# Optimization experiments

Hardware: AMD Instinct MI355X
Metric: run time of the kernel (lower is better)

Reference implementation:

```python
import jax, jax.numpy as jnp
import numpy as np

B = 4096
T = 66            # total_char_ids = 51 + 8 + 6 + 1
EMB = 128
ITEM_EMB = 64     # emb_dim // 2
NUM_ITEMS = 287
ITEMS_IN_GAME = 70  # 7 * 10
N_SCREEN = 24
N_MINI = 40
CONT = 32


def _unique_ids(key, batch, n):
    keys = jax.random.split(key, batch)
    return jax.vmap(lambda k: jax.random.permutation(k, T)[:n])(keys).astype(jnp.int32)


def setup_inputs() -> dict:
    key = jax.random.key(0)
    ks = jax.random.split(key, 16)
    inp = {
        "continuous_f": jax.random.normal(ks[0], (B, CONT), jnp.float32),
        "screen_feats": jax.random.uniform(ks[1], (B, N_SCREEN, 4), jnp.float32),
        "minimap_feats": jax.random.uniform(ks[2], (B, N_MINI, 2), jnp.float32),
        "char_emb": jax.random.normal(ks[3], (T, EMB), jnp.float32) * 0.02,
        "item_emb": jax.random.normal(ks[4], (NUM_ITEMS, ITEM_EMB), jnp.float32) * 0.02,
        "Ws1": jax.random.normal(ks[5], (EMB + 4, EMB), jnp.float32) * 0.05,
        "bs1": jnp.zeros((EMB,), jnp.float32),
        "Ws2": jax.random.normal(ks[6], (EMB, EMB), jnp.float32) * 0.05,
        "bs2": jnp.zeros((EMB,), jnp.float32),
        "Wm1": jax.random.normal(ks[7], (EMB + 2, EMB), jnp.float32) * 0.05,
        "bm1": jnp.zeros((EMB,), jnp.float32),
        "Wm2": jax.random.normal(ks[8], (EMB, EMB), jnp.float32) * 0.05,
        "bm2": jnp.zeros((EMB,), jnp.float32),
        "screen_ids": _unique_ids(ks[9], B, N_SCREEN),
        "minimap_ids": _unique_ids(ks[10], B, N_MINI),
        "items": jax.random.randint(ks[11], (B, ITEMS_IN_GAME), 0, NUM_ITEMS, jnp.int32),
    }
    return inp


def reference(continuous_f, screen_feats, minimap_feats, char_emb, item_emb,
              Ws1, bs1, Ws2, bs2, Wm1, bm1, Wm2, bm2,
              screen_ids, minimap_ids, items):
    b = continuous_f.shape[0]
    rows = jnp.arange(b)[:, None]

    # scatter detections by char id into fixed [T, .] buffers (vectorized over batch)
    scr = jnp.zeros((b, T, 4), screen_feats.dtype).at[rows, screen_ids].set(screen_feats)
    mini = jnp.zeros((b, T, 2), minimap_feats.dtype).at[rows, minimap_ids].set(minimap_feats)

    # item embedding lookup -> [b, 70*64]
    item_flat = item_emb[items].reshape(b, -1)

    base = jnp.broadcast_to(char_emb, (b, T, EMB))  # all char ids embedded

    def mlp(x, W1, b1, W2, b2):
        h = jax.nn.relu(jnp.einsum('btf,fh->bth', x, W1) + b1)
        return jnp.einsum('bth,hk->btk', h, W2) + b2

    screen_out = mlp(jnp.concatenate([base, scr], axis=-1), Ws1, bs1, Ws2, bs2)
    mini_out = mlp(jnp.concatenate([base, mini], axis=-1), Wm1, bm1, Wm2, bm2)

    obs = jnp.concatenate(
        [continuous_f, screen_out.reshape(b, -1), mini_out.reshape(b, -1), item_flat],
        axis=-1)  # [b, 32 + 66*128 + 66*128 + 70*64] = [b, 21408]
    return obs
```

## Files before the change

### kernel.cpp

```cpp
#include <hip/hip_runtime.h>
#include <stdint.h>

#define BDIM 256
#define PDIM 512
#define T_   66
#define EMB  128
#define NS   24
#define NM   40
#define NBS  42
#define NBM  26
#define NI   70
#define CONT 32
#define OUTW 21408

typedef __attribute__((ext_vector_type(4))) float f32x4;
typedef __attribute__((ext_vector_type(8))) unsigned short u16x8;
typedef __attribute__((ext_vector_type(8))) __bf16 bf16x8;

static __device__ __forceinline__ unsigned short f2bf(float x) {
  union { float f; unsigned u; } v; v.f = x;
  unsigned r = (v.u + 0x7FFFu + ((v.u >> 16) & 1u)) >> 16;
  return (unsigned short)r;
}

static __device__ __forceinline__ f32x4 mfma16(u16x8 a, u16x8 b, f32x4 c) {
  return __builtin_amdgcn_mfma_f32_16x16x32_bf16(
      __builtin_bit_cast(bf16x8, a), __builtin_bit_cast(bf16x8, b), c, 0, 0, 0);
}

__global__ __launch_bounds__(PDIM) void precomp(
    const float* __restrict__ char_emb,
    const float* __restrict__ Ws1, const float* __restrict__ bs1,
    const float* __restrict__ Ws2, const float* __restrict__ bs2,
    const float* __restrict__ Wm1, const float* __restrict__ bm1,
    const float* __restrict__ Wm2, const float* __restrict__ bm2,
    float* __restrict__ base_h_s, float* __restrict__ base_h_m,
    float* __restrict__ base_out_s, float* __restrict__ base_out_m,
    unsigned short* __restrict__ w2s_swz, unsigned short* __restrict__ w2m_swz) {
  const int bb = blockIdx.x, tid = threadIdx.x;
  if (bb < T_) {
    const int t = bb;
    const int quarter = tid >> 7;
    const int col = tid & 127;
    const int mlp = quarter & 1;
    const int kh = quarter >> 1;
    const float* W1 = mlp ? Wm1 : Ws1;
    const float* W2 = mlp ? Wm2 : Ws2;
    const float* b1 = mlp ? bm1 : bs1;
    const float* b2 = mlp ? bm2 : bs2;
    float* bh = mlp ? base_h_m : base_h_s;
    float* bo = mlp ? base_out_m : base_out_s;
    __shared__ float part[4][EMB];
    __shared__ float h[2][EMB];
    float acc = 0.f;
#pragma unroll 8
    for (int f = kh * 64; f < kh * 64 + 64; ++f)
      acc += char_emb[t * EMB + f] * W1[f * EMB + col];
    part[quarter][col] = acc;
    __syncthreads();
    if (tid < 256) {
      const float v = b1[col] + part[mlp][col] + part[2 + mlp][col];
      bh[t * EMB + col] = v;
      h[mlp][col] = fmaxf(v, 0.f);
    }
    __syncthreads();
    float acc2 = 0.f;
#pragma unroll 8
    for (int i = kh * 64; i < kh * 64 + 64; ++i)
      acc2 += h[mlp][i] * W2[i * EMB + col];
    part[quarter][col] = acc2;
    __syncthreads();
    if (tid < 256)
      bo[t * EMB + col] = b2[col] + part[mlp][col] + part[2 + mlp][col];
  } else {
    const int mlp = bb - T_;
    const float* W2 = mlp ? Wm2 : Ws2;
    unsigned short* dst = mlp ? w2m_swz : w2s_swz;
    for (int idx = tid; idx < 8 * 4 * 64 * 8; idx += PDIM) {
      const int e = idx & 7, lane = (idx >> 3) & 63, kk = (idx >> 9) & 3, n = idx >> 11;
      const int k = kk * 32 + (lane >> 4) * 8 + e;
      const int col = n * 16 + (lane & 15);
      dst[idx] = f2bf(W2[k * EMB + col]);
    }
  }
}

__global__ __launch_bounds__(BDIM, 5) void fused(
    const float* __restrict__ contf,
    const float* __restrict__ sfeat,
    const float* __restrict__ mfeat,
    const float* __restrict__ item_emb,
    const float* __restrict__ Ws1,
    const float* __restrict__ bs2,
    const float* __restrict__ Wm1,
    const float* __restrict__ bm2,
    const int* __restrict__ sids,
    const int* __restrict__ mids,
    const int* __restrict__ items,
    const float* __restrict__ base_h_s, const float* __restrict__ base_h_m,
    const float* __restrict__ base_out_s, const float* __restrict__ base_out_m,
    const unsigned short* __restrict__ w2s_swz, const unsigned short* __restrict__ w2m_swz,
    float* __restrict__ out) {
  const int bid = blockIdx.x, tid = threadIdx.x;
  const int b = bid >> 1;

  __shared__ int s_id[NS], m_id[NM];
  __shared__ float s_f[NS * 4], m_f[NM * 2];
  __shared__ u16x8 h_frag[5 * 4 * 64];
  __shared__ int s_map[T_], m_map[T_];
  __shared__ int listS[T_], listM[T_], s_item[NI];
  __shared__ int cntS, cntM;

  float* outS = out + (size_t)b * OUTW + CONT;
  float* outM = outS + T_ * EMB;

  if (bid & 1) {
    if (tid < NS) s_id[tid] = sids[b * NS + tid];
    if (tid < NM) m_id[tid] = mids[b * NM + tid];
    if (tid < NS * 4) s_f[tid] = sfeat[b * NS * 4 + tid];
    if (tid < NM * 2) m_f[tid] = mfeat[b * NM * 2 + tid];
    __syncthreads();

    for (int u = tid; u < 5 * 4 * 64; u += BDIM) {
      const int lane = u & 63, kk = (u >> 6) & 3, tile = u >> 8;
      const int g = lane >> 4, r = lane & 15;
      const int k0 = kk * 32 + g * 8;
      const bool scr = tile < 2;
      const int j = scr ? tile * 16 + r : (tile - 2) * 16 + r;
      const int nd = scr ? NS : NM;
      float v[8];
      if (j < nd) {
        const int t = scr ? s_id[j] : m_id[j];
        const float* bh = (scr ? base_h_s : base_h_m) + t * EMB + k0;
#pragma unroll
        for (int e = 0; e < 8; ++e) v[e] = bh[e];
        if (scr) {
          const float* fp = &s_f[j * 4];
#pragma unroll
          for (int c = 0; c < 4; ++c) {
            const float fc = fp[c];
            const float* wp = Ws1 + (128 + c) * EMB + k0;
#pragma unroll
            for (int e = 0; e < 8; ++e) v[e] += fc * wp[e];
          }
        } else {
          const float* fp = &m_f[j * 2];
#pragma unroll
          for (int c = 0; c < 2; ++c) {
            const float fc = fp[c];
            const float* wp = Wm1 + (128 + c) * EMB + k0;
#pragma unroll
            for (int e = 0; e < 8; ++e) v[e] += fc * wp[e];
          }
        }
#pragma unroll
        for (int e = 0; e < 8; ++e) v[e] = fmaxf(v[e], 0.f);
      } else {
#pragma unroll
        for (int e = 0; e < 8; ++e) v[e] = 0.f;
      }
      u16x8 pk;
#pragma unroll
      for (int e = 0; e < 8; ++e) pk[e] = f2bf(v[e]);
      h_frag[u] = pk;
    }
    __syncthreads();

    const int lane = tid & 63, w = tid >> 6;
    const int g = lane >> 4, r = lane & 15;
    const int n0 = w * 2;

    u16x8 bb[2][4];
    float bias[2];
#pragma unroll
    for (int n = 0; n < 2; ++n) {
      bias[n] = bs2[(n0 + n) * 16 + r];
#pragma unroll
      for (int kk = 0; kk < 4; ++kk)
        bb[n][kk] = reinterpret_cast<const u16x8*>(w2s_swz)[((n0 + n) * 4 + kk) * 64 + lane];
    }
#pragma unroll
    for (int m = 0; m < 2; ++m) {
#pragma unroll
      for (int n = 0; n < 2; ++n) {
        f32x4 acc = {bias[n], bias[n], bias[n], bias[n]};
#pragma unroll
        for (int kk = 0; kk < 4; ++kk)
          acc = mfma16(h_frag[(m * 4 + kk) * 64 + lane], bb[n][kk], acc);
#pragma unroll
        for (int q = 0; q < 4; ++q) {
          const int rd = m * 16 + g * 4 + q;
          if (rd < NS) {
            const int t = s_id[rd];
            __builtin_nontemporal_store(acc[q], outS + t * EMB + (n0 + n) * 16 + r);
          }
        }
      }
    }
#pragma unroll
    for (int n = 0; n < 2; ++n) {
      bias[n] = bm2[(n0 + n) * 16 + r];
#pragma unroll
      for (int kk = 0; kk < 4; ++kk)
        bb[n][kk] = reinterpret_cast<const u16x8*>(w2m_swz)[((n0 + n) * 4 + kk) * 64 + lane];
    }
#pragma unroll
    for (int m = 0; m < 3; ++m) {
#pragma unroll
      for (int n = 0; n < 2; ++n) {
        f32x4 acc = {bias[n], bias[n], bias[n], bias[n]};
#pragma unroll
        for (int kk = 0; kk < 4; ++kk)
          acc = mfma16(h_frag[((m + 2) * 4 + kk) * 64 + lane], bb[n][kk], acc);
#pragma unroll
        for (int q = 0; q < 4; ++q) {
          const int rd = m * 16 + g * 4 + q;
          if (rd < NM) {
            const int t = m_id[rd];
            __builtin_nontemporal_store(acc[q], outM + t * EMB + (n0 + n) * 16 + r);
          }
        }
      }
    }
  } else {
    if (tid == 0) { cntS = 0; cntM = 0; }
    if (tid < T_) { s_map[tid] = -1; m_map[tid] = -1; }
    if (tid < NS) s_id[tid] = sids[b * NS + tid];
    if (tid < NM) m_id[tid] = mids[b * NM + tid];
    if (tid < NI) s_item[tid] = items[b * NI + tid];
    __syncthreads();
    if (tid < NS) s_map[s_id[tid]] = 1;
    if (tid < NM) m_map[m_id[tid]] = 1;
    __syncthreads();
    if (tid < T_ && s_map[tid] < 0) { const int p = atomicAdd(&cntS, 1); listS[p] = tid; }
    if (tid < T_ && m_map[tid] < 0) { const int p = atomicAdd(&cntM, 1); listM[p] = tid; }
    __syncthreads();

    if (tid < 8) {
      const f32x4 v = reinterpret_cast<const f32x4*>(contf + (size_t)b * CONT)[tid];
      __builtin_nontemporal_store(v, reinterpret_cast<f32x4*>(out + (size_t)b * OUTW) + tid);
    }
    for (int u = tid; u < NBS * 32; u += BDIM) {
      const int d = u >> 5, q = u & 31;
      const int t = listS[d];
      const f32x4 v = reinterpret_cast<const f32x4*>(base_out_s + t * EMB)[q];
      __builtin_nontemporal_store(v, reinterpret_cast<f32x4*>(outS + t * EMB) + q);
    }
    for (int u = tid; u < NBM * 32; u += BDIM) {
      const int d = u >> 5, q = u & 31;
      const int t = listM[d];
      const f32x4 v = reinterpret_cast<const f32x4*>(base_out_m + t * EMB)[q];
      __builtin_nontemporal_store(v, reinterpret_cast<f32x4*>(outM + t * EMB) + q);
    }
    float* outI = out + (size_t)b * OUTW + (CONT + 2 * T_ * EMB);
    for (int u = tid; u < NI * 16; u += BDIM) {
      const int j = u >> 4, q = u & 15;
      const int it = s_item[j];
      const f32x4 v = reinterpret_cast<const f32x4*>(item_emb + it * 64)[q];
      __builtin_nontemporal_store(v, reinterpret_cast<f32x4*>(outI + j * 64) + q);
    }
  }
}

extern "C" void kernel_launch(void* const* d_in, const int* in_sizes, int n_in,
                              void* d_out, int out_size, void* d_ws, size_t ws_size,
                              hipStream_t stream) {
  const float* contf    = (const float*)d_in[0];
  const float* sfeat    = (const float*)d_in[1];
  const float* mfeat    = (const float*)d_in[2];
  const float* char_emb = (const float*)d_in[3];
  const float* item_emb = (const float*)d_in[4];
  const float* Ws1 = (const float*)d_in[5];
  const float* bs1 = (const float*)d_in[6];
  const float* Ws2 = (const float*)d_in[7];
  const float* bs2 = (const float*)d_in[8];
  const float* Wm1 = (const float*)d_in[9];
  const float* bm1 = (const float*)d_in[10];
  const float* Wm2 = (const float*)d_in[11];
  const float* bm2 = (const float*)d_in[12];
  const int* sids  = (const int*)d_in[13];
  const int* mids  = (const int*)d_in[14];
  const int* items = (const int*)d_in[15];
  float* out = (float*)d_out;

  const int B = in_sizes[0] / CONT;

  char* ws = (char*)d_ws;
  float* base_h_s   = (float*)(ws + 0);
  float* base_h_m   = (float*)(ws + 33792);
  float* base_out_s = (float*)(ws + 67584);
  float* base_out_m = (float*)(ws + 101376);
  unsigned short* w2s = (unsigned short*)(ws + 135168);
  unsigned short* w2m = (unsigned short*)(ws + 167936);

  precomp<<<T_ + 2, PDIM, 0, stream>>>(char_emb, Ws1, bs1, Ws2, bs2, Wm1, bm1, Wm2, bm2,
                                       base_h_s, base_h_m, base_out_s, base_out_m, w2s, w2m);
  fused<<<2 * B, BDIM, 0, stream>>>(contf, sfeat, mfeat, item_emb, Ws1, bs2, Wm1, bm2,
                                    sids, mids, items,
                                    base_h_s, base_h_m, base_out_s, base_out_m, w2s, w2m, out);
}
```

Before: 122.4 us.

## Process four samples per block with double-buffered metadata and hoisted W2 fragments

Replaces the two-blocks-per-sample split (MLP block and copy block) with one block handling four consecutive samples. Per-sample ids and features are double-buffered in shared memory, so loading and building the next sample overlaps the stores of the current one, and the W2 MFMA fragments and biases are loaded into registers once per block. The base-row fill now checks a per-char map instead of using an atomic-built list. This cuts launch count and repeated weight loads but gives 4x fewer blocks, more registers (the occupancy hint was removed), and serialised work within each block.

```diff
diff --git a/kernel.cpp b/kernel.cpp
--- a/kernel.cpp
+++ b/kernel.cpp
@@ -3,12 +3,11 @@
 
 #define BDIM 256
 #define PDIM 512
+#define SPB  4
 #define T_   66
 #define EMB  128
 #define NS   24
 #define NM   40
-#define NBS  42
-#define NBM  26
 #define NI   70
 #define CONT 32
 #define OUTW 21408
@@ -85,7 +84,7 @@
   }
 }
 
-__global__ __launch_bounds__(BDIM, 5) void fused(
+__global__ __launch_bounds__(BDIM) void fused(
     const float* __restrict__ contf,
     const float* __restrict__ sfeat,
     const float* __restrict__ mfeat,
@@ -100,42 +99,63 @@
     const float* __restrict__ base_h_s, const float* __restrict__ base_h_m,
     const float* __restrict__ base_out_s, const float* __restrict__ base_out_m,
     const unsigned short* __restrict__ w2s_swz, const unsigned short* __restrict__ w2m_swz,
-    float* __restrict__ out) {
-  const int bid = blockIdx.x, tid = threadIdx.x;
-  const int b = bid >> 1;
-
-  __shared__ int s_id[NS], m_id[NM];
-  __shared__ float s_f[NS * 4], m_f[NM * 2];
-  __shared__ u16x8 h_frag[5 * 4 * 64];
-  __shared__ int s_map[T_], m_map[T_];
-  __shared__ int listS[T_], listM[T_], s_item[NI];
-  __shared__ int cntS, cntM;
-
-  float* outS = out + (size_t)b * OUTW + CONT;
-  float* outM = outS + T_ * EMB;
-
-  if (bid & 1) {
-    if (tid < NS) s_id[tid] = sids[b * NS + tid];
-    if (tid < NM) m_id[tid] = mids[b * NM + tid];
-    if (tid < NS * 4) s_f[tid] = sfeat[b * NS * 4 + tid];
-    if (tid < NM * 2) m_f[tid] = mfeat[b * NM * 2 + tid];
-    __syncthreads();
-
-    for (int u = tid; u < 5 * 4 * 64; u += BDIM) {
-      const int lane = u & 63, kk = (u >> 6) & 3, tile = u >> 8;
-      const int g = lane >> 4, r = lane & 15;
-      const int k0 = kk * 32 + g * 8;
+    float* __restrict__ out, int B) {
+  const int tid = threadIdx.x;
+  const int s0 = blockIdx.x * SPB;
+  const int nS = min(SPB, B - s0);
+  if (nS <= 0) return;
+
+  __shared__ u16x8 h_frag[2][5 * 4 * 64];
+  __shared__ int s_id[2][NS], m_id[2][NM], s_item[2][NI];
+  __shared__ int s_map[2][T_], m_map[2][T_];
+  __shared__ float s_f[2][NS * 4], m_f[2][NM * 2];
+
+  const int lane = tid & 63, w = tid >> 6;
+  const int g = lane >> 4, r = lane & 15;
+  const int n0 = w * 2;
+
+  u16x8 bS[2][4], bM[2][4];
+  float biasS[2], biasM[2];
+#pragma unroll
+  for (int n = 0; n < 2; ++n) {
+    biasS[n] = bs2[(n0 + n) * 16 + r];
+    biasM[n] = bm2[(n0 + n) * 16 + r];
+#pragma unroll
+    for (int kk = 0; kk < 4; ++kk) {
+      bS[n][kk] = reinterpret_cast<const u16x8*>(w2s_swz)[((n0 + n) * 4 + kk) * 64 + lane];
+      bM[n][kk] = reinterpret_cast<const u16x8*>(w2m_swz)[((n0 + n) * 4 + kk) * 64 + lane];
+    }
+  }
+
+  auto LOADMETA = [&](int s, int buf) {
+    if (tid < T_) { s_map[buf][tid] = -1; m_map[buf][tid] = -1; }
+    if (tid < NS) s_id[buf][tid] = sids[s * NS + tid];
+    if (tid < NM) m_id[buf][tid] = mids[s * NM + tid];
+    if (tid < NI) s_item[buf][tid] = items[s * NI + tid];
+    if (tid < NS * 4) s_f[buf][tid] = sfeat[s * NS * 4 + tid];
+    if (tid < NM * 2) m_f[buf][tid] = mfeat[s * NM * 2 + tid];
+  };
+
+  auto BUILD = [&](int buf) {
+    if (tid < NS) s_map[buf][s_id[buf][tid]] = tid;
+    if (tid < NM) m_map[buf][m_id[buf][tid]] = tid;
+#pragma unroll
+    for (int it = 0; it < 5; ++it) {
+      const int u = it * BDIM + tid;
+      const int ln = u & 63, kk = (u >> 6) & 3, tile = u >> 8;
+      const int gg = ln >> 4, rr = ln & 15;
+      const int k0 = kk * 32 + gg * 8;
       const bool scr = tile < 2;
-      const int j = scr ? tile * 16 + r : (tile - 2) * 16 + r;
+      const int j = scr ? tile * 16 + rr : (tile - 2) * 16 + rr;
       const int nd = scr ? NS : NM;
       float v[8];
       if (j < nd) {
-        const int t = scr ? s_id[j] : m_id[j];
+        const int t = scr ? s_id[buf][j] : m_id[buf][j];
         const float* bh = (scr ? base_h_s : base_h_m) + t * EMB + k0;
 #pragma unroll
         for (int e = 0; e < 8; ++e) v[e] = bh[e];
         if (scr) {
-          const float* fp = &s_f[j * 4];
+          const float* fp = &s_f[buf][j * 4];
 #pragma unroll
           for (int c = 0; c < 4; ++c) {
             const float fc = fp[c];
@@ -144,7 +164,7 @@
             for (int e = 0; e < 8; ++e) v[e] += fc * wp[e];
           }
         } else {
-          const float* fp = &m_f[j * 2];
+          const float* fp = &m_f[buf][j * 2];
 #pragma unroll
           for (int c = 0; c < 2; ++c) {
             const float fc = fp[c];
@@ -162,102 +182,87 @@
       u16x8 pk;
 #pragma unroll
       for (int e = 0; e < 8; ++e) pk[e] = f2bf(v[e]);
-      h_frag[u] = pk;
-    }
-    __syncthreads();
-
-    const int lane = tid & 63, w = tid >> 6;
-    const int g = lane >> 4, r = lane & 15;
-    const int n0 = w * 2;
-
-    u16x8 bb[2][4];
-    float bias[2];
-#pragma unroll
-    for (int n = 0; n < 2; ++n) {
-      bias[n] = bs2[(n0 + n) * 16 + r];
-#pragma unroll
-      for (int kk = 0; kk < 4; ++kk)
-        bb[n][kk] = reinterpret_cast<const u16x8*>(w2s_swz)[((n0 + n) * 4 + kk) * 64 + lane];
-    }
+      h_frag[buf][u] = pk;
+    }
+  };
+
+  auto STOREALL = [&](int b, int buf) {
+    float* outS = out + (size_t)b * OUTW + CONT;
+    float* outM = outS + T_ * EMB;
 #pragma unroll
     for (int m = 0; m < 2; ++m) {
 #pragma unroll
       for (int n = 0; n < 2; ++n) {
-        f32x4 acc = {bias[n], bias[n], bias[n], bias[n]};
+        f32x4 acc = {biasS[n], biasS[n], biasS[n], biasS[n]};
 #pragma unroll
         for (int kk = 0; kk < 4; ++kk)
-          acc = mfma16(h_frag[(m * 4 + kk) * 64 + lane], bb[n][kk], acc);
+          acc = mfma16(h_frag[buf][(m * 4 + kk) * 64 + lane], bS[n][kk], acc);
 #pragma unroll
         for (int q = 0; q < 4; ++q) {
           const int rd = m * 16 + g * 4 + q;
           if (rd < NS) {
-            const int t = s_id[rd];
+            const int t = s_id[buf][rd];
             __builtin_nontemporal_store(acc[q], outS + t * EMB + (n0 + n) * 16 + r);
           }
         }
       }
     }
 #pragma unroll
-    for (int n = 0; n < 2; ++n) {
-      bias[n] = bm2[(n0 + n) * 16 + r];
-#pragma unroll
-      for (int kk = 0; kk < 4; ++kk)
-        bb[n][kk] = reinterpret_cast<const u16x8*>(w2m_swz)[((n0 + n) * 4 + kk) * 64 + lane];
-    }
-#pragma unroll
     for (int m = 0; m < 3; ++m) {
 #pragma unroll
       for (int n = 0; n < 2; ++n) {
-        f32x4 acc = {bias[n], bias[n], bias[n], bias[n]};
+        f32x4 acc = {biasM[n], biasM[n], biasM[n], biasM[n]};
 #pragma unroll
         for (int kk = 0; kk < 4; ++kk)
-          acc = mfma16(h_frag[((m + 2) * 4 + kk) * 64 + lane], bb[n][kk], acc);
+          acc = mfma16(h_frag[buf][((m + 2) * 4 + kk) * 64 + lane], bM[n][kk], acc);
 #pragma unroll
         for (int q = 0; q < 4; ++q) {
           const int rd = m * 16 + g * 4 + q;
           if (rd < NM) {
-            const int t = m_id[rd];
+            const int t = m_id[buf][rd];
             __builtin_nontemporal_store(acc[q], outM + t * EMB + (n0 + n) * 16 + r);
           }
         }
       }
     }
-  } else {
-    if (tid == 0) { cntS = 0; cntM = 0; }
-    if (tid < T_) { s_map[tid] = -1; m_map[tid] = -1; }
-    if (tid < NS) s_id[tid] = sids[b * NS + tid];
-    if (tid < NM) m_id[tid] = mids[b * NM + tid];
-    if (tid < NI) s_item[tid] = items[b * NI + tid];
-    __syncthreads();
-    if (tid < NS) s_map[s_id[tid]] = 1;
-    if (tid < NM) m_map[m_id[tid]] = 1;
-    __syncthreads();
-    if (tid < T_ && s_map[tid] < 0) { const int p = atomicAdd(&cntS, 1); listS[p] = tid; }
-    if (tid < T_ && m_map[tid] < 0) { const int p = atomicAdd(&cntM, 1); listM[p] = tid; }
-    __syncthreads();
-
+    for (int u = tid; u < T_ * 32; u += BDIM) {
+      const int t = u >> 5, q = u & 31;
+      if (s_map[buf][t] < 0) {
+        const f32x4 v = reinterpret_cast<const f32x4*>(base_out_s + t * EMB)[q];
+        __builtin_nontemporal_store(v, reinterpret_cast<f32x4*>(outS + t * EMB) + q);
+      }
+    }
+    for (int u = tid; u < T_ * 32; u += BDIM) {
+      const int t = u >> 5, q = u & 31;
+      if (m_map[buf][t] < 0) {
+        const f32x4 v = reinterpret_cast<const f32x4*>(base_out_m + t * EMB)[q];
+        __builtin_nontemporal_store(v, reinterpret_cast<f32x4*>(outM + t * EMB) + q);
+      }
+    }
+    float* outI = out + (size_t)b * OUTW + (CONT + 2 * T_ * EMB);
+    for (int u = tid; u < NI * 16; u += BDIM) {
+      const int j = u >> 4, q = u & 15;
+      const int it = s_item[buf][j];
+      const f32x4 v = reinterpret_cast<const f32x4*>(item_emb + it * 64)[q];
+      __builtin_nontemporal_store(v, reinterpret_cast<f32x4*>(outI + j * 64) + q);
+    }
     if (tid < 8) {
       const f32x4 v = reinterpret_cast<const f32x4*>(contf + (size_t)b * CONT)[tid];
       __builtin_nontemporal_store(v, reinterpret_cast<f32x4*>(out + (size_t)b * OUTW) + tid);
     }
-    for (int u = tid; u < NBS * 32; u += BDIM) {
-      const int d = u >> 5, q = u & 31;
-      const int t = listS[d];
-      const f32x4 v = reinterpret_cast<const f32x4*>(base_out_s + t * EMB)[q];
-      __builtin_nontemporal_store(v, reinterpret_cast<f32x4*>(outS + t * EMB) + q);
-    }
-    for (int u = tid; u < NBM * 32; u += BDIM) {
-      const int d = u >> 5, q = u & 31;
-      const int t = listM[d];
-      const f32x4 v = reinterpret_cast<const f32x4*>(base_out_m + t * EMB)[q];
-      __builtin_nontemporal_store(v, reinterpret_cast<f32x4*>(outM + t * EMB) + q);
-    }
-    float* outI = out + (size_t)b * OUTW + (CONT + 2 * T_ * EMB);
-    for (int u = tid; u < NI * 16; u += BDIM) {
-      const int j = u >> 4, q = u & 15;
-      const int it = s_item[j];
-      const f32x4 v = reinterpret_cast<const f32x4*>(item_emb + it * 64)[q];
-      __builtin_nontemporal_store(v, reinterpret_cast<f32x4*>(outI + j * 64) + q);
+  };
+
+  LOADMETA(s0, 0);
+  __syncthreads();
+  BUILD(0);
+  for (int i = 0; i < nS; ++i) {
+    const int cur = i & 1;
+    __syncthreads();
+    if (i + 1 < nS) LOADMETA(s0 + i + 1, cur ^ 1);
+    STOREALL(s0 + i, cur);
+    if (i + 1 < nS) {
+      __syncthreads();
+      BUILD(cur ^ 1);
     }
   }
 }
@@ -295,7 +300,8 @@
 
   precomp<<<T_ + 2, PDIM, 0, stream>>>(char_emb, Ws1, bs1, Ws2, bs2, Wm1, bm1, Wm2, bm2,
                                        base_h_s, base_h_m, base_out_s, base_out_m, w2s, w2m);
-  fused<<<2 * B, BDIM, 0, stream>>>(contf, sfeat, mfeat, item_emb, Ws1, bs2, Wm1, bm2,
-                                    sids, mids, items,
-                                    base_h_s, base_h_m, base_out_s, base_out_m, w2s, w2m, out);
-}
+  fused<<<(B + SPB - 1) / SPB, BDIM, 0, stream>>>(
+      contf, sfeat, mfeat, item_emb, Ws1, bs2, Wm1, bm2,
+      sids, mids, items,
+      base_h_s, base_h_m, base_out_s, base_out_m, w2s, w2m, out, B);
+}
```

Result: faster. 104.7 us (-14.5%).
